# Kernel tuning notes

Measured on AMD Instinct MI355X. Metric: run time of the kernel, lower is better.

Reference implementation:

```python
import jax, jax.numpy as jnp
import numpy as np
from jax import lax

H = 512  # hidden_size

def run_layer(x_seq, m_seq, wih, bih, whh, reverse):
    """One directional highway-LSTM layer.
    x_seq: [T,B,in], m_seq: [T,B,1], wih: [6H,in], bih: [6H], whh: [5H,H].
    Returns (out [T,B,H], (h_T, c_T))."""
    T, B, _ = x_seq.shape
    # input projection for all timesteps at once: [T,B,6H]
    xproj = jnp.einsum('tbi,gi->tbg', x_seq, wih) + bih
    h0 = jnp.zeros((B, H), dtype=x_seq.dtype)
    c0 = jnp.zeros((B, H), dtype=x_seq.dtype)

    def step(carry, inp):
        h, c = carry
        xp, m = inp  # xp: [B,6H], m: [B,1]
        preact = h @ whh.T + xp[:, :5 * H]
        i, f, o, t, j = jnp.split(preact, 5, axis=1)
        i = jax.nn.sigmoid(i)
        f = jax.nn.sigmoid(f + 1.0)
        o = jax.nn.sigmoid(o)
        t = jax.nn.sigmoid(t)
        j = jnp.tanh(j)
        k = xp[:, 5 * H:]
        c_new = f * c + i * j
        c_new = m * c_new + (1.0 - m) * c
        h_new = t * o * jnp.tanh(c_new) + (1.0 - t) * k
        h_new = m * h_new + (1.0 - m) * h
        return (h_new, c_new), h_new

    (hT, cT), outs = lax.scan(step, (h0, c0), (xproj, m_seq), reverse=reverse)
    return outs, (hT, cT)


def setup_inputs() -> dict:
    key = jax.random.key(0)
    ks = jax.random.split(key, 16)
    T, B, IN = 512, 32, 512
    s_ih = 1.0 / np.sqrt(IN)
    s_hh = 1.0 / np.sqrt(H)
    d = {
        'x': jax.random.normal(ks[0], (T, B, IN), jnp.float32),
        'masks': jnp.ones((T, B, 1), jnp.float32),
    }
    i = 1
    for tag in ['f0', 'b0', 'f1', 'b1']:
        d['wih_' + tag] = jax.random.normal(ks[i], (6 * H, IN), jnp.float32) * s_ih; i += 1
        d['bih_' + tag] = jnp.zeros((6 * H,), jnp.float32)
        d['whh_' + tag] = jax.random.normal(ks[i], (5 * H, H), jnp.float32) * s_hh; i += 1
    return d


def reference(x, masks, wih_f0, bih_f0, whh_f0, wih_b0, bih_b0, whh_b0,
              wih_f1, bih_f1, whh_f1, wih_b1, bih_b1, whh_b1):
    # layer 0 forward then backward (backward consumes forward's output)
    out_f0, (hf0, cf0) = run_layer(x, masks, wih_f0, bih_f0, whh_f0, reverse=False)
    out_b0, (hb0, cb0) = run_layer(out_f0, masks, wih_b0, bih_b0, whh_b0, reverse=True)
    # layer 1: input is the backward output of layer 0
    out_f1, (hf1, cf1) = run_layer(out_b0, masks, wih_f1, bih_f1, whh_f1, reverse=False)
    out_b1, (hb1, cb1) = run_layer(out_f1, masks, wih_b1, bih_b1, whh_b1, reverse=True)
    h_n = jnp.stack([hf0, hb0, hf1, hb1], axis=0)  # [4,B,H]
    c_n = jnp.stack([cf0, cb0, cf1, cb1], axis=0)
    return out_b1, h_n, c_n
```

## Files before the change

kernel.cpp:

```cpp
#include <hip/hip_runtime.h>
#include <hip/hip_bf16.h>
#include <stdint.h>
#include <stddef.h>
#include <math.h>

#define HH 512
#define TT 512
#define BB 32
#define XH 3072
#define GH 2560
#define NWG 32
#define UPW 16
#define NGRP 2
#define RPG 16
#define KCH 16
#define HSK 520
#define POISON64 0xFFFFFFFFFFFFFFFFULL
#define SCOPE __HIP_MEMORY_SCOPE_AGENT
#define WGSC  __HIP_MEMORY_SCOPE_WORKGROUP

typedef __attribute__((ext_vector_type(8))) short bf16x8;
typedef __attribute__((ext_vector_type(4))) float f32x4;
typedef unsigned long long u64;

__device__ __forceinline__ float bf2f(unsigned short u){
  union{float f; unsigned int i;} v; v.i = ((unsigned int)u)<<16; return v.f;
}
__device__ __forceinline__ unsigned short f2bf(float f){
  union{float f; unsigned int i;} v; v.f=f;
  unsigned int x=v.i;
  return (unsigned short)((x + 0x7FFFu + ((x>>16)&1u))>>16);
}
__device__ __forceinline__ float sigm(float x){ return 1.f/(1.f+__expf(-x)); }
__device__ __forceinline__ float tanh_f(float x){ return 1.f - 2.f/(__expf(2.f*x)+1.f); }

__global__ void fill_sentinel_f(float* out, int n, float v){
  int i = blockIdx.x*blockDim.x + threadIdx.x;
  int stride = gridDim.x*blockDim.x;
  for (; i < n; i += stride) out[i] = v;
}

__global__ void conv_f2bf(const float* __restrict__ in, unsigned short* __restrict__ out, int n){
  int i = (blockIdx.x*blockDim.x + threadIdx.x)*4;
  int stride = gridDim.x*blockDim.x*4;
  for (; i < n; i += stride){
    float4 v = *(const float4*)(in + i);
    ushort4 o; o.x=f2bf(v.x); o.y=f2bf(v.y); o.z=f2bf(v.z); o.w=f2bf(v.w);
    *(ushort4*)(out + i) = o;
  }
}

#define BM 128
#define BN 128
#define BKK 32

__global__ __launch_bounds__(256)
void gemm_bt(const unsigned short* __restrict__ A, const unsigned short* __restrict__ Bt,
             const float* __restrict__ bias, unsigned short* __restrict__ C,
             int M, int N, int K)
{
  __shared__ unsigned short Alds[BM*BKK];
  __shared__ unsigned short Blds[BN*BKK];
  const int tid = threadIdx.x;
  const int lane = tid & 63;
  const int w = tid >> 6;
  const int gm = blockIdx.y, gn = blockIdx.x;
  const int wm = (w>>1)*64, wn = (w&1)*64;
  const int l15 = lane & 15, l4 = lane >> 4;
  f32x4 acc[4][4] = {};
  for (int k0 = 0; k0 < K; k0 += BKK){
    __syncthreads();
    #pragma unroll
    for (int it = 0; it < 2; ++it){
      int id2 = it*256 + tid;
      int row = id2 >> 2, kc = (id2 & 3)*8;
      *(bf16x8*)&Alds[row*BKK + kc] = *(const bf16x8*)(A + (size_t)(gm*BM+row)*K + k0 + kc);
      *(bf16x8*)&Blds[row*BKK + kc] = *(const bf16x8*)(Bt + (size_t)(gn*BN+row)*K + k0 + kc);
    }
    __syncthreads();
    bf16x8 af[4], bfv[4];
    #pragma unroll
    for (int i=0;i<4;i++) af[i]  = *(const bf16x8*)&Alds[(wm + i*16 + l15)*BKK + l4*8];
    #pragma unroll
    for (int j=0;j<4;j++) bfv[j] = *(const bf16x8*)&Blds[(wn + j*16 + l15)*BKK + l4*8];
    #pragma unroll
    for (int i=0;i<4;i++)
      #pragma unroll
      for (int j=0;j<4;j++)
        acc[i][j] = __builtin_amdgcn_mfma_f32_16x16x32_bf16(af[i], bfv[j], acc[i][j], 0,0,0);
  }
  #pragma unroll
  for (int i=0;i<4;i++){
    int row0 = gm*BM + wm + i*16 + l4*4;
    #pragma unroll
    for (int j=0;j<4;j++){
      int col = gn*BN + wn + j*16 + l15;
      float bz = bias[col];
      #pragma unroll
      for (int r=0;r<4;r++)
        C[(size_t)(row0+r)*N + col] = f2bf(acc[i][j][r] + bz);
    }
  }
}

__global__ __launch_bounds__(512)
void lstm_scan_v13(const unsigned short* __restrict__ xp,
                   const float* __restrict__ whh,
                   const float* __restrict__ masks,
                   unsigned short* __restrict__ ab,
                   float* __restrict__ outF,
                   float* __restrict__ hT_out, float* __restrict__ cT_out,
                   int* __restrict__ flags,
                   int reverse)
{
  __shared__ __align__(16) unsigned short hs[KCH*HSK];
  __shared__ float pre[5][RPG][17];
  __shared__ unsigned short xps[2][6][RPG][16];
  __shared__ float mlds[2][RPG];
  __shared__ __align__(8) unsigned short pwl[RPG*16];
  __shared__ int go_l;

  const int gid = blockIdx.x & 1;
  const int wgi = blockIdx.x >> 1;
  const int tid = threadIdx.x, wv = tid >> 6, lane = tid & 63;
  const int l15 = lane & 15, l4 = lane >> 4;
  const int u0 = wgi*UPW;
  const int r0 = gid*RPG;
  int* gflags = flags + gid*NWG*16;
  int* myflag = gflags + wgi*16;

  if (tid == 0) go_l = 0;

  bf16x8 Bhi[KCH], Blo[KCH];
  if (wv < 5){
    const float* wrow = whh + ((size_t)(wv*HH + u0 + l15))*HH + l4*8;
    #pragma unroll
    for (int kc = 0; kc < KCH; ++kc){
      float4 v0 = *(const float4*)(wrow + kc*32);
      float4 v1 = *(const float4*)(wrow + kc*32 + 4);
      float vv[8] = {v0.x,v0.y,v0.z,v0.w,v1.x,v1.y,v1.z,v1.w};
      bf16x8 hh, ll;
      #pragma unroll
      for (int j = 0; j < 8; ++j){
        unsigned short hb = f2bf(vv[j]);
        hh[j] = (short)hb;
        ll[j] = (short)f2bf(vv[j] - bf2f(hb));
      }
      Bhi[kc] = hh; Blo[kc] = ll;
    }
  }

  if (wv == 6){
    const int t0 = reverse ? (TT-1) : 0;
    #pragma unroll
    for (int it = 0; it < 3; ++it){
      int p = it*64 + lane;
      int half = p & 1, pg = p >> 1;
      int g = pg % 6, row = pg / 6;
      *(uint4*)&xps[0][g][row][half*8] =
        *(const uint4*)(xp + ((size_t)t0*BB + r0 + row)*XH + g*HH + u0 + half*8);
    }
    if (lane < RPG) mlds[0][lane] = masks[t0*BB + r0 + lane];
  }

  const int r4 = lane >> 4, uu = lane & 15;
  float c_st[4] = {0,0,0,0}, h_st[4] = {0,0,0,0};
  __syncthreads();

  for (int s = 0; s < TT; ++s){
    const int t = reverse ? (TT-1-s) : s;
    if (s > 0){
      const int tp = reverse ? (t+1) : (t-1);
      const u64* src = (const u64*)(ab + ((size_t)tp*BB + r0)*HH);
      u64 v[4];
      #pragma unroll
      for (int it = 0; it < 4; ++it)
        v[it] = __hip_atomic_load(&src[it*512 + tid], __ATOMIC_RELAXED, SCOPE);
      if (wv == 7){
        for (;;){
          int fv = (lane < NWG)
            ? __hip_atomic_load(gflags + lane*16, __ATOMIC_RELAXED, SCOPE) : s;
          if (__all(fv >= s)) break;
          __builtin_amdgcn_s_sleep(1);
        }
        if (lane == 0) __hip_atomic_store(&go_l, s, __ATOMIC_RELAXED, WGSC);
      } else {
        while (__hip_atomic_load(&go_l, __ATOMIC_RELAXED, WGSC) < s){}
      }
      int rounds = 0;
      for (;;){
        bool bad = false;
        #pragma unroll
        for (int it = 0; it < 4; ++it){
          if (v[it] == POISON64){
            v[it] = __hip_atomic_load(&src[it*512 + tid], __ATOMIC_RELAXED, SCOPE);
            bad = true;
          }
        }
        if (!bad) break;
        if (++rounds > 2) __builtin_amdgcn_s_sleep(1);
      }
      #pragma unroll
      for (int it = 0; it < 4; ++it){
        int j = it*512 + tid;
        int r = j >> 7, ww = j & 127;
        int kc = ww >> 3, q4 = (ww >> 1) & 3, half = ww & 1;
        *(u64*)&hs[kc*HSK + (q4*16 + r)*8 + half*4] = v[it];
      }
    }
    __syncthreads();
    if (s > 0 && wv < 5){
      f32x4 a1 = {0.f,0.f,0.f,0.f}, a2 = {0.f,0.f,0.f,0.f};
      #pragma unroll
      for (int kc = 0; kc < KCH; ++kc){
        bf16x8 A = *(const bf16x8*)&hs[kc*HSK + lane*8];
        a1 = __builtin_amdgcn_mfma_f32_16x16x32_bf16(A, Bhi[kc], a1, 0,0,0);
        a2 = __builtin_amdgcn_mfma_f32_16x16x32_bf16(A, Blo[kc], a2, 0,0,0);
      }
      #pragma unroll
      for (int r = 0; r < 4; ++r) pre[wv][l4*4 + r][l15] = a1[r] + a2[r];
    }
    if (wv == 6 && s+1 < TT){
      const int t1 = reverse ? (t-1) : (t+1);
      const int nb = (s+1) & 1;
      #pragma unroll
      for (int it = 0; it < 3; ++it){
        int p = it*64 + lane;
        int half = p & 1, pg = p >> 1;
        int g = pg % 6, row = pg / 6;
        *(uint4*)&xps[nb][g][row][half*8] =
          *(const uint4*)(xp + ((size_t)t1*BB + r0 + row)*XH + g*HH + u0 + half*8);
      }
      if (lane < RPG) mlds[nb][lane] = masks[t1*BB + r0 + lane];
    }
    __syncthreads();
    if (wv == 5){
      const int sb = s & 1;
      float hvals[4];
      #pragma unroll
      for (int i = 0; i < 4; ++i){
        const int row = r4 + i*4;
        float p0=0,p1=0,p2=0,p3=0,p4=0;
        if (s > 0){
          p0 = pre[0][row][uu]; p1 = pre[1][row][uu]; p2 = pre[2][row][uu];
          p3 = pre[3][row][uu]; p4 = pre[4][row][uu];
        }
        float xi = bf2f(xps[sb][0][row][uu]);
        float xf = bf2f(xps[sb][1][row][uu]);
        float xo = bf2f(xps[sb][2][row][uu]);
        float xg = bf2f(xps[sb][3][row][uu]);
        float xj = bf2f(xps[sb][4][row][uu]);
        float xk = bf2f(xps[sb][5][row][uu]);
        float mm = mlds[sb][row];
        float ig = sigm(p0 + xi);
        float fg = sigm(p1 + xf + 1.0f);
        float og = sigm(p2 + xo);
        float tg = sigm(p3 + xg);
        float jg = tanh_f(p4 + xj);
        float cn = fg*c_st[i] + ig*jg;
        cn = mm*cn + (1.f-mm)*c_st[i];
        float hn = tg*og*tanh_f(cn) + (1.f-tg)*xk;
        hn = mm*hn + (1.f-mm)*h_st[i];
        c_st[i] = cn; h_st[i] = hn;
        hvals[i] = hn;
        pwl[row*16 + uu] = f2bf(hn);
      }
      __threadfence_block();
      {
        int row = lane >> 2, q = lane & 3;
        u64 v = *(const u64*)&pwl[row*16 + q*4];
        u64* dstp = (u64*)(ab + ((size_t)t*BB + r0 + row)*HH + u0 + q*4);
        __hip_atomic_store(dstp, v, __ATOMIC_RELAXED, SCOPE);
      }
      if (lane == 0)
        __hip_atomic_store(myflag, s+1, __ATOMIC_RELAXED, SCOPE);
      if (outF){
        #pragma unroll
        for (int i = 0; i < 4; ++i)
          outF[((size_t)t*BB + r0 + r4 + i*4)*HH + u0 + uu] = hvals[i];
      }
    }
  }
  if (wv == 5){
    #pragma unroll
    for (int i = 0; i < 4; ++i){
      int row = r0 + r4 + i*4;
      hT_out[(size_t)row*HH + u0 + uu] = h_st[i];
      cT_out[(size_t)row*HH + u0 + uu] = c_st[i];
    }
  }
}

extern "C" void kernel_launch(void* const* d_in, const int* in_sizes, int n_in,
                              void* d_out, int out_size, void* d_ws, size_t ws_size,
                              hipStream_t stream)
{
  const float* x = nullptr; const float* masks = nullptr;
  const float* wih[4] = {}; const float* bih[4] = {}; const float* whh[4] = {};
  int nw = 0, nb = 0, nh = 0;
  for (int i = 0; i < n_in; ++i){
    const int sz = in_sizes[i];
    const float* p = (const float*)d_in[i];
    if      (sz == TT*BB*HH){ if (!x) x = p; }
    else if (sz == TT*BB)   { if (!masks) masks = p; }
    else if (sz == XH*HH)   { if (nw < 4) wih[nw++] = p; }
    else if (sz == XH)      { if (nb < 4) bih[nb++] = p; }
    else if (sz == GH*HH)   { if (nh < 4) whh[nh++] = p; }
  }
  float* out = (float*)d_out;
  if (!x || !masks || nw != 4 || nb != 4 || nh != 4){
    fill_sentinel_f<<<512, 256, 0, stream>>>(out, out_size, 777.0f);
    return;
  }

  char* ws = (char*)d_ws;
  size_t off = 0;
  auto alloc = [&](size_t bytes)->void*{
    void* p = ws + off; off += (bytes + 255) & ~(size_t)255; return p;
  };
  unsigned short* xbf   = (unsigned short*)alloc((size_t)TT*BB*HH*2);
  unsigned short* ab0   = (unsigned short*)alloc((size_t)TT*BB*HH*2);
  unsigned short* ab1   = (unsigned short*)alloc((size_t)TT*BB*HH*2);
  unsigned short* wbf   = (unsigned short*)alloc((size_t)XH*HH*2);
  unsigned short* xproj = (unsigned short*)alloc((size_t)TT*BB*XH*2);
  int*            flags = (int*)alloc((size_t)4*NGRP*NWG*16*4);

  (void)hipMemsetAsync(flags, 0, (size_t)4*NGRP*NWG*16*4, stream);

  const int thr = 256;
  auto cgrid = [&](int n){ int g = (n/4 + thr - 1)/thr; return g > 2048 ? 2048 : g; };
  conv_f2bf<<<cgrid(TT*BB*HH), thr, 0, stream>>>(x, xbf, TT*BB*HH);

  float* hn = out + (size_t)TT*BB*HH;
  float* cn = hn + (size_t)4*BB*HH;

  unsigned short* ab[2] = {ab0, ab1};

  for (int L = 0; L < 4; ++L){
    const int rev = L & 1;
    unsigned short* cur  = ab[L & 1];
    const unsigned short* prev = (L == 0) ? xbf : ab[(L+1) & 1];
    conv_f2bf<<<cgrid(XH*HH), thr, 0, stream>>>(wih[L], wbf, XH*HH);
    gemm_bt<<<dim3(XH/BN, (TT*BB)/BM), 256, 0, stream>>>(
        prev, wbf, bih[L], xproj, TT*BB, XH, HH);
    (void)hipMemsetAsync(cur, 0xFF, (size_t)TT*BB*HH*2, stream);

    lstm_scan_v13<<<NGRP*NWG, 512, 0, stream>>>(
        xproj, whh[L], masks, cur,
        (L == 3) ? out : nullptr,
        hn + (size_t)L*BB*HH, cn + (size_t)L*BB*HH,
        flags + (size_t)L*NGRP*NWG*16,
        rev);
  }
}
```

Before: 8.395 ms.

## Merge batch groups into 16 workgroups with single fp16 MFMA recurrence

The recurrent scan now runs on 16 workgroups, each covering all 32 batch rows and 32 hidden units, instead of 64 workgroups split across two batch groups. The recurrent weights become a single fp16 operand, replacing the bf16 hi/lo split that doubled the MFMA count. The h exchange moves to a separate fp16 buffer while a bf16 copy feeds the next layer's GEMM. Two waves compute the cell update, with input projections prefetched into registers instead of LDS. This cuts MFMA work and the number of flag pollers per step, but each workgroup loads twice the h tile, only 16 CUs run the scan, and fp16 weights plus fp16 h may lose precision compared to the hi/lo bf16 scheme.

```diff
diff --git a/kernel.cpp b/kernel.cpp
--- a/kernel.cpp
+++ b/kernel.cpp
@@ -9,10 +9,8 @@
 #define BB 32
 #define XH 3072
 #define GH 2560
-#define NWG 32
-#define UPW 16
-#define NGRP 2
-#define RPG 16
+#define NWG 16
+#define UPW 32
 #define KCH 16
 #define HSK 520
 #define POISON64 0xFFFFFFFFFFFFFFFFULL
@@ -20,6 +18,7 @@
 #define WGSC  __HIP_MEMORY_SCOPE_WORKGROUP
 
 typedef __attribute__((ext_vector_type(8))) short bf16x8;
+typedef __attribute__((ext_vector_type(8))) _Float16 f16x8;
 typedef __attribute__((ext_vector_type(4))) float f32x4;
 typedef unsigned long long u64;
 
@@ -104,82 +103,77 @@
 }
 
 __global__ __launch_bounds__(512)
-void lstm_scan_v13(const unsigned short* __restrict__ xp,
+void lstm_scan_v14(const unsigned short* __restrict__ xp,
                    const float* __restrict__ whh,
                    const float* __restrict__ masks,
-                   unsigned short* __restrict__ ab,
+                   unsigned short* __restrict__ hx,
+                   unsigned short* __restrict__ abf,
                    float* __restrict__ outF,
                    float* __restrict__ hT_out, float* __restrict__ cT_out,
                    int* __restrict__ flags,
                    int reverse)
 {
-  __shared__ __align__(16) unsigned short hs[KCH*HSK];
-  __shared__ float pre[5][RPG][17];
-  __shared__ unsigned short xps[2][6][RPG][16];
-  __shared__ float mlds[2][RPG];
-  __shared__ __align__(8) unsigned short pwl[RPG*16];
+  __shared__ __align__(16) unsigned short hs[2][KCH*HSK];
+  __shared__ float pre[5][32][33];
+  __shared__ __align__(8) unsigned short pwl[2][16*32];
   __shared__ int go_l;
 
-  const int gid = blockIdx.x & 1;
-  const int wgi = blockIdx.x >> 1;
+  const int wgi = blockIdx.x;
   const int tid = threadIdx.x, wv = tid >> 6, lane = tid & 63;
   const int l15 = lane & 15, l4 = lane >> 4;
   const int u0 = wgi*UPW;
-  const int r0 = gid*RPG;
-  int* gflags = flags + gid*NWG*16;
-  int* myflag = gflags + wgi*16;
-
   if (tid == 0) go_l = 0;
 
-  bf16x8 Bhi[KCH], Blo[KCH];
+  f16x8 Bv[2][16];
   if (wv < 5){
-    const float* wrow = whh + ((size_t)(wv*HH + u0 + l15))*HH + l4*8;
-    #pragma unroll
-    for (int kc = 0; kc < KCH; ++kc){
-      float4 v0 = *(const float4*)(wrow + kc*32);
-      float4 v1 = *(const float4*)(wrow + kc*32 + 4);
-      float vv[8] = {v0.x,v0.y,v0.z,v0.w,v1.x,v1.y,v1.z,v1.w};
-      bf16x8 hh, ll;
-      #pragma unroll
-      for (int j = 0; j < 8; ++j){
-        unsigned short hb = f2bf(vv[j]);
-        hh[j] = (short)hb;
-        ll[j] = (short)f2bf(vv[j] - bf2f(hb));
-      }
-      Bhi[kc] = hh; Blo[kc] = ll;
-    }
-  }
-
-  if (wv == 6){
+    #pragma unroll
+    for (int n = 0; n < 2; ++n){
+      const float* wrow = whh + ((size_t)(wv*HH + u0 + n*16 + l15))*HH + l4*8;
+      #pragma unroll
+      for (int kc = 0; kc < KCH; ++kc){
+        float4 v0 = *(const float4*)(wrow + kc*32);
+        float4 v1 = *(const float4*)(wrow + kc*32 + 4);
+        f16x8 f;
+        f[0]=(_Float16)v0.x; f[1]=(_Float16)v0.y; f[2]=(_Float16)v0.z; f[3]=(_Float16)v0.w;
+        f[4]=(_Float16)v1.x; f[5]=(_Float16)v1.y; f[6]=(_Float16)v1.z; f[7]=(_Float16)v1.w;
+        Bv[n][kc] = f;
+      }
+    }
+  }
+
+  const int p = wv - 5;
+  const int rbase = p*16;
+  const int r4 = lane >> 4, uu = lane & 15;
+  float c_st[4][2], h_st[4][2];
+  unsigned short cx[4][6][2];
+  float cmask[4];
+  if (wv == 5 || wv == 6){
+    #pragma unroll
+    for (int i = 0; i < 4; ++i){
+      c_st[i][0]=0.f; c_st[i][1]=0.f; h_st[i][0]=0.f; h_st[i][1]=0.f;
+    }
     const int t0 = reverse ? (TT-1) : 0;
     #pragma unroll
-    for (int it = 0; it < 3; ++it){
-      int p = it*64 + lane;
-      int half = p & 1, pg = p >> 1;
-      int g = pg % 6, row = pg / 6;
-      *(uint4*)&xps[0][g][row][half*8] =
-        *(const uint4*)(xp + ((size_t)t0*BB + r0 + row)*XH + g*HH + u0 + half*8);
-    }
-    if (lane < RPG) mlds[0][lane] = masks[t0*BB + r0 + lane];
-  }
-
-  const int r4 = lane >> 4, uu = lane & 15;
-  float c_st[4] = {0,0,0,0}, h_st[4] = {0,0,0,0};
+    for (int i = 0; i < 4; ++i){
+      const int row = rbase + r4 + i*4;
+      cmask[i] = masks[t0*BB + row];
+      #pragma unroll
+      for (int g = 0; g < 6; ++g){
+        const size_t base = ((size_t)t0*BB + row)*XH + g*HH + u0;
+        cx[i][g][0] = xp[base + uu];
+        cx[i][g][1] = xp[base + uu + 16];
+      }
+    }
+  }
   __syncthreads();
 
   for (int s = 0; s < TT; ++s){
     const int t = reverse ? (TT-1-s) : s;
     if (s > 0){
-      const int tp = reverse ? (t+1) : (t-1);
-      const u64* src = (const u64*)(ab + ((size_t)tp*BB + r0)*HH);
-      u64 v[4];
-      #pragma unroll
-      for (int it = 0; it < 4; ++it)
-        v[it] = __hip_atomic_load(&src[it*512 + tid], __ATOMIC_RELAXED, SCOPE);
       if (wv == 7){
         for (;;){
-          int fv = (lane < NWG)
-            ? __hip_atomic_load(gflags + lane*16, __ATOMIC_RELAXED, SCOPE) : s;
+          int fv = (lane < 32)
+            ? __hip_atomic_load(flags + lane*16, __ATOMIC_RELAXED, SCOPE) : s;
           if (__all(fv >= s)) break;
           __builtin_amdgcn_s_sleep(1);
         }
@@ -187,11 +181,17 @@
       } else {
         while (__hip_atomic_load(&go_l, __ATOMIC_RELAXED, WGSC) < s){}
       }
+      const int tp = reverse ? (t+1) : (t-1);
+      const u64* src = (const u64*)(hx + (size_t)tp*BB*HH);
+      u64 v[8];
+      #pragma unroll
+      for (int it = 0; it < 8; ++it)
+        v[it] = __hip_atomic_load(&src[it*512 + tid], __ATOMIC_RELAXED, SCOPE);
       int rounds = 0;
       for (;;){
         bool bad = false;
         #pragma unroll
-        for (int it = 0; it < 4; ++it){
+        for (int it = 0; it < 8; ++it){
           if (v[it] == POISON64){
             v[it] = __hip_atomic_load(&src[it*512 + tid], __ATOMIC_RELAXED, SCOPE);
             bad = true;
@@ -201,92 +201,100 @@
         if (++rounds > 2) __builtin_amdgcn_s_sleep(1);
       }
       #pragma unroll
-      for (int it = 0; it < 4; ++it){
+      for (int it = 0; it < 8; ++it){
         int j = it*512 + tid;
-        int r = j >> 7, ww = j & 127;
+        int rg = j >> 7, ww = j & 127;
         int kc = ww >> 3, q4 = (ww >> 1) & 3, half = ww & 1;
-        *(u64*)&hs[kc*HSK + (q4*16 + r)*8 + half*4] = v[it];
+        *(u64*)&hs[rg >> 4][kc*HSK + (q4*16 + (rg & 15))*8 + half*4] = v[it];
       }
     }
     __syncthreads();
     if (s > 0 && wv < 5){
-      f32x4 a1 = {0.f,0.f,0.f,0.f}, a2 = {0.f,0.f,0.f,0.f};
+      f32x4 acc[2][2] = {};
       #pragma unroll
       for (int kc = 0; kc < KCH; ++kc){
-        bf16x8 A = *(const bf16x8*)&hs[kc*HSK + lane*8];
-        a1 = __builtin_amdgcn_mfma_f32_16x16x32_bf16(A, Bhi[kc], a1, 0,0,0);
-        a2 = __builtin_amdgcn_mfma_f32_16x16x32_bf16(A, Blo[kc], a2, 0,0,0);
-      }
-      #pragma unroll
-      for (int r = 0; r < 4; ++r) pre[wv][l4*4 + r][l15] = a1[r] + a2[r];
-    }
-    if (wv == 6 && s+1 < TT){
-      const int t1 = reverse ? (t-1) : (t+1);
-      const int nb = (s+1) & 1;
-      #pragma unroll
-      for (int it = 0; it < 3; ++it){
-        int p = it*64 + lane;
-        int half = p & 1, pg = p >> 1;
-        int g = pg % 6, row = pg / 6;
-        *(uint4*)&xps[nb][g][row][half*8] =
-          *(const uint4*)(xp + ((size_t)t1*BB + r0 + row)*XH + g*HH + u0 + half*8);
-      }
-      if (lane < RPG) mlds[nb][lane] = masks[t1*BB + r0 + lane];
+        f16x8 A0 = *(const f16x8*)&hs[0][kc*HSK + lane*8];
+        f16x8 A1 = *(const f16x8*)&hs[1][kc*HSK + lane*8];
+        acc[0][0] = __builtin_amdgcn_mfma_f32_16x16x32_f16(A0, Bv[0][kc], acc[0][0], 0,0,0);
+        acc[0][1] = __builtin_amdgcn_mfma_f32_16x16x32_f16(A0, Bv[1][kc], acc[0][1], 0,0,0);
+        acc[1][0] = __builtin_amdgcn_mfma_f32_16x16x32_f16(A1, Bv[0][kc], acc[1][0], 0,0,0);
+        acc[1][1] = __builtin_amdgcn_mfma_f32_16x16x32_f16(A1, Bv[1][kc], acc[1][1], 0,0,0);
+      }
+      #pragma unroll
+      for (int mt = 0; mt < 2; ++mt)
+        #pragma unroll
+        for (int n = 0; n < 2; ++n)
+          #pragma unroll
+          for (int r = 0; r < 4; ++r)
+            pre[wv][mt*16 + l4*4 + r][n*16 + l15] = acc[mt][n][r];
     }
     __syncthreads();
-    if (wv == 5){
-      const int sb = s & 1;
-      float hvals[4];
+    if (wv == 5 || wv == 6){
       #pragma unroll
       for (int i = 0; i < 4; ++i){
-        const int row = r4 + i*4;
-        float p0=0,p1=0,p2=0,p3=0,p4=0;
-        if (s > 0){
-          p0 = pre[0][row][uu]; p1 = pre[1][row][uu]; p2 = pre[2][row][uu];
-          p3 = pre[3][row][uu]; p4 = pre[4][row][uu];
+        const int row = rbase + r4 + i*4;
+        const float mm = cmask[i];
+        #pragma unroll
+        for (int uc = 0; uc < 2; ++uc){
+          const int u = uu + uc*16;
+          float p0=0,p1=0,p2=0,p3=0,p4=0;
+          if (s > 0){
+            p0 = pre[0][row][u]; p1 = pre[1][row][u]; p2 = pre[2][row][u];
+            p3 = pre[3][row][u]; p4 = pre[4][row][u];
+          }
+          float ig = sigm(p0 + bf2f(cx[i][0][uc]));
+          float fg = sigm(p1 + bf2f(cx[i][1][uc]) + 1.0f);
+          float og = sigm(p2 + bf2f(cx[i][2][uc]));
+          float tg = sigm(p3 + bf2f(cx[i][3][uc]));
+          float jg = tanh_f(p4 + bf2f(cx[i][4][uc]));
+          float xk = bf2f(cx[i][5][uc]);
+          float cn = fg*c_st[i][uc] + ig*jg;
+          cn = mm*cn + (1.f-mm)*c_st[i][uc];
+          float hn = tg*og*tanh_f(cn) + (1.f-tg)*xk;
+          hn = mm*hn + (1.f-mm)*h_st[i][uc];
+          c_st[i][uc] = cn; h_st[i][uc] = hn;
+          _Float16 hf = (_Float16)hn;
+          pwl[p][(r4 + i*4)*32 + u] = __builtin_bit_cast(unsigned short, hf);
+          abf[((size_t)t*BB + row)*HH + u0 + u] = f2bf(hn);
+          if (outF) outF[((size_t)t*BB + row)*HH + u0 + u] = hn;
         }
-        float xi = bf2f(xps[sb][0][row][uu]);
-        float xf = bf2f(xps[sb][1][row][uu]);
-        float xo = bf2f(xps[sb][2][row][uu]);
-        float xg = bf2f(xps[sb][3][row][uu]);
-        float xj = bf2f(xps[sb][4][row][uu]);
-        float xk = bf2f(xps[sb][5][row][uu]);
-        float mm = mlds[sb][row];
-        float ig = sigm(p0 + xi);
-        float fg = sigm(p1 + xf + 1.0f);
-        float og = sigm(p2 + xo);
-        float tg = sigm(p3 + xg);
-        float jg = tanh_f(p4 + xj);
-        float cn = fg*c_st[i] + ig*jg;
-        cn = mm*cn + (1.f-mm)*c_st[i];
-        float hn = tg*og*tanh_f(cn) + (1.f-tg)*xk;
-        hn = mm*hn + (1.f-mm)*h_st[i];
-        c_st[i] = cn; h_st[i] = hn;
-        hvals[i] = hn;
-        pwl[row*16 + uu] = f2bf(hn);
       }
       __threadfence_block();
-      {
-        int row = lane >> 2, q = lane & 3;
-        u64 v = *(const u64*)&pwl[row*16 + q*4];
-        u64* dstp = (u64*)(ab + ((size_t)t*BB + r0 + row)*HH + u0 + q*4);
+      #pragma unroll
+      for (int k2 = 0; k2 < 2; ++k2){
+        int idx = lane*2 + k2;
+        int rloc = idx >> 3, q = idx & 7;
+        u64 v = *(const u64*)&pwl[p][rloc*32 + q*4];
+        u64* dstp = (u64*)(hx + ((size_t)t*BB + rbase + rloc)*HH + u0 + q*4);
         __hip_atomic_store(dstp, v, __ATOMIC_RELAXED, SCOPE);
       }
       if (lane == 0)
-        __hip_atomic_store(myflag, s+1, __ATOMIC_RELAXED, SCOPE);
-      if (outF){
+        __hip_atomic_store(flags + (wgi*2 + p)*16, s+1, __ATOMIC_RELAXED, SCOPE);
+      if (s+1 < TT){
+        const int t1 = reverse ? (t-1) : (t+1);
         #pragma unroll
-        for (int i = 0; i < 4; ++i)
-          outF[((size_t)t*BB + r0 + r4 + i*4)*HH + u0 + uu] = hvals[i];
-      }
-    }
-  }
-  if (wv == 5){
+        for (int i = 0; i < 4; ++i){
+          const int row = rbase + r4 + i*4;
+          cmask[i] = masks[t1*BB + row];
+          #pragma unroll
+          for (int g = 0; g < 6; ++g){
+            const size_t base = ((size_t)t1*BB + row)*XH + g*HH + u0;
+            cx[i][g][0] = xp[base + uu];
+            cx[i][g][1] = xp[base + uu + 16];
+          }
+        }
+      }
+    }
+  }
+  if (wv == 5 || wv == 6){
     #pragma unroll
     for (int i = 0; i < 4; ++i){
-      int row = r0 + r4 + i*4;
-      hT_out[(size_t)row*HH + u0 + uu] = h_st[i];
-      cT_out[(size_t)row*HH + u0 + uu] = c_st[i];
+      const int row = rbase + r4 + i*4;
+      #pragma unroll
+      for (int uc = 0; uc < 2; ++uc){
+        hT_out[(size_t)row*HH + u0 + uu + uc*16] = h_st[i][uc];
+        cT_out[(size_t)row*HH + u0 + uu + uc*16] = c_st[i][uc];
+      }
     }
   }
 }
@@ -319,13 +327,13 @@
     void* p = ws + off; off += (bytes + 255) & ~(size_t)255; return p;
   };
   unsigned short* xbf   = (unsigned short*)alloc((size_t)TT*BB*HH*2);
-  unsigned short* ab0   = (unsigned short*)alloc((size_t)TT*BB*HH*2);
-  unsigned short* ab1   = (unsigned short*)alloc((size_t)TT*BB*HH*2);
+  unsigned short* abf   = (unsigned short*)alloc((size_t)TT*BB*HH*2);
+  unsigned short* hx    = (unsigned short*)alloc((size_t)TT*BB*HH*2);
   unsigned short* wbf   = (unsigned short*)alloc((size_t)XH*HH*2);
   unsigned short* xproj = (unsigned short*)alloc((size_t)TT*BB*XH*2);
-  int*            flags = (int*)alloc((size_t)4*NGRP*NWG*16*4);
-
-  (void)hipMemsetAsync(flags, 0, (size_t)4*NGRP*NWG*16*4, stream);
+  int*            flags = (int*)alloc((size_t)4*32*16*4);
+
+  (void)hipMemsetAsync(flags, 0, (size_t)4*32*16*4, stream);
 
   const int thr = 256;
   auto cgrid = [&](int n){ int g = (n/4 + thr - 1)/thr; return g > 2048 ? 2048 : g; };
@@ -334,22 +342,19 @@
   float* hn = out + (size_t)TT*BB*HH;
   float* cn = hn + (size_t)4*BB*HH;
 
-  unsigned short* ab[2] = {ab0, ab1};
-
   for (int L = 0; L < 4; ++L){
     const int rev = L & 1;
-    unsigned short* cur  = ab[L & 1];
-    const unsigned short* prev = (L == 0) ? xbf : ab[(L+1) & 1];
+    const unsigned short* prev = (L == 0) ? xbf : abf;
     conv_f2bf<<<cgrid(XH*HH), thr, 0, stream>>>(wih[L], wbf, XH*HH);
     gemm_bt<<<dim3(XH/BN, (TT*BB)/BM), 256, 0, stream>>>(
         prev, wbf, bih[L], xproj, TT*BB, XH, HH);
-    (void)hipMemsetAsync(cur, 0xFF, (size_t)TT*BB*HH*2, stream);
-
-    lstm_scan_v13<<<NGRP*NWG, 512, 0, stream>>>(
-        xproj, whh[L], masks, cur,
+    (void)hipMemsetAsync(hx, 0xFF, (size_t)TT*BB*HH*2, stream);
+
+    lstm_scan_v14<<<NWG, 512, 0, stream>>>(
+        xproj, whh[L], masks, hx, abf,
         (L == 3) ? out : nullptr,
         hn + (size_t)L*BB*HH, cn + (size_t)L*BB*HH,
-        flags + (size_t)L*NGRP*NWG*16,
+        flags + (size_t)L*32*16,
         rev);
   }
 }
```

New measurement: 19.44 ms. 132% more time.
